# Optimization experiments

Hardware: AMD Instinct MI355X
Metric: run time of the kernel (lower is better)

## Reference

```python
import jax, jax.numpy as jnp
import numpy as np

RES = (32, 32, 32)   # S, H, W
WS = 4               # window size (cubic)
SHIFT = 2            # shift size
NH = 6               # num heads
C = 192              # dim
EPS = 1e-5


def _rel_pos_index(ws):
    coords = np.stack(np.meshgrid(np.arange(ws), np.arange(ws), np.arange(ws), indexing='ij'))
    cf = coords.reshape(3, -1)                      # (3, N)
    rc = (cf[:, :, None] - cf[:, None, :]).transpose(1, 2, 0).astype(np.int64)  # (N,N,3)
    rc[..., 0] += ws - 1
    rc[..., 1] += ws - 1
    rc[..., 2] += ws - 1
    rc[..., 0] *= 3 * ws - 1
    rc[..., 1] *= 2 * ws - 1
    return rc.sum(-1)                               # (N, N)

_RPI = jnp.asarray(_rel_pos_index(WS))


def _ln(x, g, b):
    m = jnp.mean(x, axis=-1, keepdims=True)
    v = jnp.mean(jnp.square(x - m), axis=-1, keepdims=True)
    return (x - m) * jax.lax.rsqrt(v + EPS) * g + b


def setup_inputs():
    key = jax.random.key(0)
    ks = jax.random.split(key, 12)
    B, L = 2, RES[0] * RES[1] * RES[2]
    nW, N = 512, WS ** 3
    Hd = 4 * C
    p = lambda k, s: jax.random.normal(k, s, jnp.float32) * 0.02
    return {
        'x': jax.random.normal(ks[0], (B, L, C), jnp.float32),
        'mask_matrix': jax.random.normal(ks[1], (nW, N, N), jnp.float32),
        'skip': jax.random.normal(ks[2], (B, L, C), jnp.float32),
        'x_up': jax.random.normal(ks[3], (B, L, C), jnp.float32),
        'norm1_g': jnp.ones((C,), jnp.float32), 'norm1_b': jnp.zeros((C,), jnp.float32),
        'kv_w': p(ks[4], (C, 2 * C)), 'kv_b': jnp.zeros((2 * C,), jnp.float32),
        'rpb_table': p(ks[5], ((2 * WS - 1) ** 3, NH)),
        'proj_w': p(ks[6], (C, C)), 'proj_b': jnp.zeros((C,), jnp.float32),
        'norm2_g': jnp.ones((C,), jnp.float32), 'norm2_b': jnp.zeros((C,), jnp.float32),
        'fc1_w': p(ks[7], (C, Hd)), 'fc1_b': jnp.zeros((Hd,), jnp.float32),
        'fc2_w': p(ks[8], (Hd, C)), 'fc2_b': jnp.zeros((C,), jnp.float32),
    }


def reference(x, mask_matrix, skip, x_up, norm1_g, norm1_b, kv_w, kv_b, rpb_table,
              proj_w, proj_b, norm2_g, norm2_b, fc1_w, fc1_b, fc2_w, fc2_b):
    B, L, _ = x.shape
    S, H, W = RES
    ws, N = WS, WS ** 3
    hd = C // NH
    scale = hd ** -0.5

    sn = _ln(skip, norm1_g, norm1_b).reshape(B, S, H, W, C)
    qn = _ln(x_up, norm1_g, norm1_b).reshape(B, S, H, W, C)
    # cyclic shift (shift_size > 0)
    sn = jnp.roll(sn, (-SHIFT, -SHIFT, -SHIFT), axis=(1, 2, 3))
    qn = jnp.roll(qn, (-SHIFT, -SHIFT, -SHIFT), axis=(1, 2, 3))

    def part(t):  # window partition -> (B*nW, N, C)
        t = t.reshape(B, S // ws, ws, H // ws, ws, W // ws, ws, C)
        return t.transpose(0, 1, 3, 5, 2, 4, 6, 7).reshape(-1, N, C)

    skw, qw = part(sn), part(qn)
    B_ = skw.shape[0]

    kv = (skw @ kv_w + kv_b).reshape(B_, N, 2, NH, hd)
    k = kv[:, :, 0].transpose(0, 2, 1, 3)   # (B_, NH, N, hd)
    v = kv[:, :, 1].transpose(0, 2, 1, 3)
    q = qw.reshape(B_, N, NH, hd).transpose(0, 2, 1, 3) * scale

    attn = jnp.einsum('bhqd,bhkd->bhqk', q, k)
    rpb = rpb_table[_RPI.reshape(-1)].reshape(N, N, NH).transpose(2, 0, 1)  # (NH, N, N)
    attn = attn + rpb[None]
    nW = mask_matrix.shape[0]
    attn = attn.reshape(B, nW, NH, N, N) + mask_matrix[None, :, None]
    attn = jax.nn.softmax(attn.reshape(B_, NH, N, N), axis=-1)

    out = jnp.einsum('bhqk,bhkd->bhqd', attn, v).transpose(0, 2, 1, 3).reshape(B_, N, C)
    out = out @ proj_w + proj_b

    # window reverse
    out = out.reshape(B, S // ws, H // ws, W // ws, ws, ws, ws, C)
    out = out.transpose(0, 1, 4, 2, 5, 3, 6, 7).reshape(B, S, H, W, C)
    out = jnp.roll(out, (SHIFT, SHIFT, SHIFT), axis=(1, 2, 3)).reshape(B, L, C)

    x = x + out
    h = _ln(x, norm2_g, norm2_b)
    h = jax.nn.gelu(h @ fc1_w + fc1_b, approximate=False) @ fc2_w + fc2_b
    return x + h
```

## Files before the change

kernel.cpp:

```cpp
#include <hip/hip_runtime.h>
#include <math.h>

typedef unsigned short u16;
typedef __bf16 bf16x8 __attribute__((ext_vector_type(8)));
typedef float f32x4 __attribute__((ext_vector_type(4)));
typedef unsigned short u16x8 __attribute__((ext_vector_type(8)));

#define SHIFT 2

static __device__ __forceinline__ f32x4 mfma16(bf16x8 a, bf16x8 b, f32x4 c) {
  return __builtin_amdgcn_mfma_f32_16x16x32_bf16(a, b, c, 0, 0, 0);
}
static __device__ __forceinline__ u16 f2bf(float f) {
  unsigned u = __builtin_bit_cast(unsigned, f);
  unsigned r = u + 0x7fffu + ((u >> 16) & 1u);
  return (u16)(r >> 16);
}
static __device__ __forceinline__ float bf2f(u16 u) {
  unsigned v = (unsigned)u << 16;
  return __builtin_bit_cast(float, v);
}
static __device__ __forceinline__ void stage16(const u16* g, u16* lbase, int lane) {
#if __has_builtin(__builtin_amdgcn_global_load_lds)
  __builtin_amdgcn_global_load_lds(
      (const __attribute__((address_space(1))) unsigned int*)g,
      (__attribute__((address_space(3))) unsigned int*)lbase, 16, 0, 0);
#else
  *(u16x8*)(lbase + lane * 8) = *(const u16x8*)g;
#endif
}

#define OFF_KVWT  ((size_t)0)
#define OFF_PRWT  (OFF_KVWT + 384*192*2)
#define OFF_FC1WT (OFF_PRWT + 192*192*2)
#define OFF_FC2WT (OFF_FC1WT + 768*192*2)
#define OFF_SKW   (OFF_FC2WT + 192*768*2)
#define OFF_QW    (OFF_SKW + (size_t)65536*192*2)
#define OFF_KVB   (OFF_QW + (size_t)65536*192*2)
#define OFF_HN    (OFF_KVB + (size_t)65536*384*2)
#define OFF_PO    (OFF_HN + (size_t)65536*192*2)

__global__ __launch_bounds__(256) void k_prep(
    const float* __restrict__ kv_w, const float* __restrict__ proj_w,
    const float* __restrict__ fc1_w, const float* __restrict__ fc2_w,
    u16* __restrict__ kvT, u16* __restrict__ prT,
    u16* __restrict__ f1T, u16* __restrict__ f2T) {
  int i = blockIdx.x * 256 + threadIdx.x;
  if (i < 192 * 384) kvT[(i % 384) * 192 + i / 384] = f2bf(kv_w[i]);
  if (i < 192 * 192) prT[(i % 192) * 192 + i / 192] = f2bf(proj_w[i]);
  if (i < 192 * 768) f1T[(i % 768) * 192 + i / 768] = f2bf(fc1_w[i]);
  if (i < 768 * 192) f2T[(i % 192) * 768 + i / 192] = f2bf(fc2_w[i]);
}

__global__ __launch_bounds__(256) void k_ln_part(
    const float* __restrict__ skip, const float* __restrict__ x_up,
    const float* __restrict__ gam, const float* __restrict__ bet,
    u16* __restrict__ skw, u16* __restrict__ qw) {
  int row = blockIdx.x * 4 + (threadIdx.x >> 6);
  int lane = threadIdx.x & 63;
  const float* sp = skip + (size_t)row * 192;
  const float* qp = x_up + (size_t)row * 192;
  float sv[3], qv[3], ss = 0.f, qs = 0.f;
#pragma unroll
  for (int j = 0; j < 3; j++) {
    sv[j] = sp[lane + 64 * j]; qv[j] = qp[lane + 64 * j];
    ss += sv[j]; qs += qv[j];
  }
#pragma unroll
  for (int m = 1; m < 64; m <<= 1) { ss += __shfl_xor(ss, m, 64); qs += __shfl_xor(qs, m, 64); }
  float sm = ss * (1.f / 192.f), qm = qs * (1.f / 192.f);
  float s2 = 0.f, q2 = 0.f;
#pragma unroll
  for (int j = 0; j < 3; j++) { float d = sv[j] - sm; s2 += d * d; d = qv[j] - qm; q2 += d * d; }
#pragma unroll
  for (int m = 1; m < 64; m <<= 1) { s2 += __shfl_xor(s2, m, 64); q2 += __shfl_xor(q2, m, 64); }
  float sr = rsqrtf(s2 * (1.f / 192.f) + 1e-5f), qr = rsqrtf(q2 * (1.f / 192.f) + 1e-5f);
  int b = row >> 15, l = row & 32767;
  int s = l >> 10, h = (l >> 5) & 31, w = l & 31;
  int s_ = (s - SHIFT) & 31, h_ = (h - SHIFT) & 31, w_ = (w - SHIFT) & 31;
  int wIdx = ((s_ >> 2) * 8 + (h_ >> 2)) * 8 + (w_ >> 2);
  int n = ((s_ & 3) * 4 + (h_ & 3)) * 4 + (w_ & 3);
  size_t orow = ((size_t)(b * 512 + wIdx) * 64 + n) * 192;
  const float scale = 0.17677669529663687f;
#pragma unroll
  for (int j = 0; j < 3; j++) {
    int cc = lane + 64 * j;
    float gg = gam[cc], bb = bet[cc];
    skw[orow + cc] = f2bf((sv[j] - sm) * sr * gg + bb);
    qw[orow + cc]  = f2bf(((qv[j] - qm) * qr * gg + bb) * scale);
  }
}

__global__ __launch_bounds__(256) void k_kv(
    const u16* __restrict__ A, const u16* __restrict__ BT,
    const float* __restrict__ bias, u16* __restrict__ outh) {
  __shared__ u16 lds[(128 + 128) * 64];
  int mb = blockIdx.x, nb = blockIdx.y;
  int tid = threadIdx.x, w = tid >> 6, l = tid & 63;
  int wr = w >> 1, wc = w & 1, g = l >> 4, c = l & 15;
  f32x4 acc[4][4] = {};
  for (int ks = 0; ks < 3; ks++) {
    if (ks) __syncthreads();
    int k0 = ks * 64;
#pragma unroll
    for (int i = 0; i < 4; i++) {
      int s = w * 4 + i;
      stage16(&A[(size_t)(mb * 128 + s * 8 + (l >> 3)) * 192 + k0 + (l & 7) * 8],
              &lds[s * 512], l);
      stage16(&BT[(size_t)(nb * 128 + s * 8 + (l >> 3)) * 192 + k0 + (l & 7) * 8],
              &lds[8192 + s * 512], l);
    }
    __syncthreads();
#pragma unroll
    for (int kk = 0; kk < 2; kk++) {
      bf16x8 a[4];
#pragma unroll
      for (int m = 0; m < 4; m++)
        a[m] = *(const bf16x8*)&lds[(wr * 64 + m * 16 + c) * 64 + kk * 32 + g * 8];
#pragma unroll
      for (int n = 0; n < 4; n++) {
        bf16x8 b = *(const bf16x8*)&lds[8192 + (wc * 64 + n * 16 + c) * 64 + kk * 32 + g * 8];
#pragma unroll
        for (int m = 0; m < 4; m++) acc[m][n] = mfma16(a[m], b, acc[m][n]);
      }
    }
  }
#pragma unroll
  for (int m = 0; m < 4; m++)
#pragma unroll
    for (int n = 0; n < 4; n++)
#pragma unroll
      for (int r = 0; r < 4; r++) {
        int row = mb * 128 + wr * 64 + m * 16 + g * 4 + r;
        int col = nb * 128 + wc * 64 + n * 16 + c;
        outh[(size_t)row * 384 + col] = f2bf(acc[m][n][r] + bias[col]);
      }
}

__global__ __launch_bounds__(384) void k_attn_mega(
    const u16* __restrict__ qw, const u16* __restrict__ kvb,
    const float* __restrict__ rpb, const float* __restrict__ mask,
    const u16* __restrict__ prT, const float* __restrict__ proj_b,
    const float* __restrict__ x, const float* __restrict__ g2,
    const float* __restrict__ b2, u16* __restrict__ hn, u16* __restrict__ po) {
  __shared__ u16 lv[64 * 200];
  __shared__ u16 lp[6][16 * 72];
  __shared__ u16 lo[64 * 200];
  __shared__ float pf[64 * 16];
  int b_ = blockIdx.x, wIdx = b_ & 511;
  int tid = threadIdx.x, l = tid & 63, wv = tid >> 6, g = l >> 4, c = l & 15;
#pragma unroll
  for (int i = 0; i < 4; i++) {
    int cid = tid + i * 384;
    int row = cid / 24, ch = cid % 24;
    *(u16x8*)&lv[row * 200 + ch * 8] =
        *(const u16x8*)&kvb[((size_t)b_ * 64 + row) * 384 + 192 + ch * 8];
  }
  __syncthreads();
  int h = wv;
  bf16x8 qa[4], kb[4];
#pragma unroll
  for (int m = 0; m < 4; m++)
    qa[m] = *(const bf16x8*)&qw[((size_t)b_ * 64 + m * 16 + c) * 192 + h * 32 + g * 8];
#pragma unroll
  for (int n = 0; n < 4; n++)
    kb[n] = *(const bf16x8*)&kvb[((size_t)b_ * 64 + n * 16 + c) * 384 + h * 32 + g * 8];
  f32x4 acc[4][4] = {};
#pragma unroll
  for (int m = 0; m < 4; m++)
#pragma unroll
    for (int n = 0; n < 4; n++) acc[m][n] = mfma16(qa[m], kb[n], acc[m][n]);
  bf16x8 vb[2][2];
#pragma unroll
  for (int kk = 0; kk < 2; kk++)
#pragma unroll
    for (int nd = 0; nd < 2; nd++) {
      union { u16 u[8]; bf16x8 v; } bb;
#pragma unroll
      for (int j = 0; j < 8; j++)
        bb.u[j] = lv[(kk * 32 + g * 8 + j) * 200 + h * 32 + nd * 16 + c];
      vb[kk][nd] = bb.v;
    }
  const float* mrow = mask + (size_t)wIdx * 4096;
  f32x4 oacc[4][2] = {};
#pragma unroll
  for (int m = 0; m < 4; m++) {
#pragma unroll
    for (int r = 0; r < 4; r++) {
      int qr = m * 16 + g * 4 + r;
      int qs = qr >> 4, qh = (qr >> 2) & 3, qx = qr & 3;
      float vals[4];
#pragma unroll
      for (int n = 0; n < 4; n++) {
        int kc = n * 16 + c;
        int ks = kc >> 4, kh = (kc >> 2) & 3, kx = kc & 3;
        int idx = (qs - ks + 3) * 11 + (qh - kh + 3) * 7 + (qx - kx + 3);
        vals[n] = acc[m][n][r] + rpb[idx * 6 + h] + mrow[qr * 64 + kc];
      }
      float mx = fmaxf(fmaxf(vals[0], vals[1]), fmaxf(vals[2], vals[3]));
#pragma unroll
      for (int mm = 1; mm < 16; mm <<= 1) mx = fmaxf(mx, __shfl_xor(mx, mm, 64));
      float sum = 0.f;
#pragma unroll
      for (int n = 0; n < 4; n++) { vals[n] = __expf(vals[n] - mx); sum += vals[n]; }
#pragma unroll
      for (int mm = 1; mm < 16; mm <<= 1) sum += __shfl_xor(sum, mm, 64);
      float inv = 1.f / sum;
#pragma unroll
      for (int n = 0; n < 4; n++)
        lp[h][(g * 4 + r) * 72 + n * 16 + c] = f2bf(vals[n] * inv);
    }
#pragma unroll
    for (int kk = 0; kk < 2; kk++) {
      bf16x8 pa = *(const bf16x8*)&lp[h][c * 72 + kk * 32 + g * 8];
#pragma unroll
      for (int nd = 0; nd < 2; nd++) oacc[m][nd] = mfma16(pa, vb[kk][nd], oacc[m][nd]);
    }
  }
#pragma unroll
  for (int m = 0; m < 4; m++)
#pragma unroll
    for (int nd = 0; nd < 2; nd++)
#pragma unroll
      for (int r = 0; r < 4; r++)
        lo[(m * 16 + g * 4 + r) * 200 + h * 32 + nd * 16 + c] = f2bf(oacc[m][nd][r]);
  __syncthreads();
  f32x4 pacc[4][2] = {};
#pragma unroll
  for (int ks = 0; ks < 6; ks++) {
    bf16x8 pa[4];
#pragma unroll
    for (int m = 0; m < 4; m++)
      pa[m] = *(const bf16x8*)&lo[(m * 16 + c) * 200 + ks * 32 + g * 8];
#pragma unroll
    for (int n = 0; n < 2; n++) {
      bf16x8 pb = *(const bf16x8*)&prT[(size_t)(wv * 32 + n * 16 + c) * 192 + ks * 32 + g * 8];
#pragma unroll
      for (int m = 0; m < 4; m++) pacc[m][n] = mfma16(pa[m], pb, pacc[m][n]);
    }
  }
  int bI = b_ >> 9;
  int wS = wIdx >> 6, wH = (wIdx >> 3) & 7, wW = wIdx & 7;
  float yv[4][2][4];
#pragma unroll
  for (int m = 0; m < 4; m++)
#pragma unroll
    for (int r = 0; r < 4; r++) {
      int tok = m * 16 + g * 4 + r;
      int inS = tok >> 4, inH = (tok >> 2) & 3, inW = tok & 3;
      int s = (wS * 4 + inS + SHIFT) & 31;
      int hh = (wH * 4 + inH + SHIFT) & 31;
      int ww = (wW * 4 + inW + SHIFT) & 31;
      size_t base = ((size_t)bI * 32768 + ((size_t)s * 32 + hh) * 32 + ww) * 192;
      float sum = 0.f, sq = 0.f;
#pragma unroll
      for (int n = 0; n < 2; n++) {
        int col = wv * 32 + n * 16 + c;
        float v = pacc[m][n][r] + proj_b[col];
        po[base + col] = f2bf(v);
        float y = v + x[base + col];
        yv[m][n][r] = y;
        sum += y; sq += y * y;
      }
#pragma unroll
      for (int mm = 1; mm < 16; mm <<= 1) { sum += __shfl_xor(sum, mm, 64); sq += __shfl_xor(sq, mm, 64); }
      if (c == 0) { pf[tok * 16 + wv] = sum; pf[tok * 16 + 8 + wv] = sq; }
    }
  __syncthreads();
#pragma unroll
  for (int m = 0; m < 4; m++)
#pragma unroll
    for (int r = 0; r < 4; r++) {
      int tok = m * 16 + g * 4 + r;
      int inS = tok >> 4, inH = (tok >> 2) & 3, inW = tok & 3;
      int s = (wS * 4 + inS + SHIFT) & 31;
      int hh = (wH * 4 + inH + SHIFT) & 31;
      int ww = (wW * 4 + inW + SHIFT) & 31;
      size_t base = ((size_t)bI * 32768 + ((size_t)s * 32 + hh) * 32 + ww) * 192;
      float su = 0.f, qu = 0.f;
#pragma unroll
      for (int w6 = 0; w6 < 6; w6++) { su += pf[tok * 16 + w6]; qu += pf[tok * 16 + 8 + w6]; }
      float mu = su * (1.f / 192.f);
      float rs = rsqrtf(qu * (1.f / 192.f) - mu * mu + 1e-5f);
#pragma unroll
      for (int n = 0; n < 2; n++) {
        int col = wv * 32 + n * 16 + c;
        hn[base + col] = f2bf((yv[m][n][r] - mu) * rs * g2[col] + b2[col]);
      }
    }
}

__global__ __launch_bounds__(256, 2) void k_mlp(
    const u16* __restrict__ hn, const u16* __restrict__ f1T,
    const u16* __restrict__ f2T, const float* __restrict__ b1,
    const float* __restrict__ b2f, const float* __restrict__ x,
    const u16* __restrict__ po, float* __restrict__ out) {
  __shared__ u16 lds[29184];
  u16* f1c = lds;
  u16* f2c = lds + 12288;
  u16* h1c = lds + 24576;
  int tid = threadIdx.x, l = tid & 63, wv = tid >> 6, g = l >> 4, c = l & 15;
  size_t tokbase = (size_t)blockIdx.x * 64;

#pragma unroll
  for (int i = 0; i < 6; i++) {
    int CI = i * 256 + wv * 64 + l;
    int row = CI / 24, chp = CI % 24;
    int sch = (chp & 24) | ((chp ^ row) & 7);
    stage16(hn + (tokbase + row) * 192 + sch * 8, f1c + (i * 256 + wv * 64) * 8, l);
  }
  __syncthreads();
  bf16x8 hb[4][6];
#pragma unroll
  for (int tf = 0; tf < 4; tf++)
#pragma unroll
    for (int ks = 0; ks < 6; ks++) {
      int ch = ks * 4 + g;
      int chp = (ch & 24) | ((ch ^ c) & 7);
      hb[tf][ks] = *(const bf16x8*)&f1c[(tf * 16 + c) * 192 + chp * 8];
    }
  f32x4 acc2[3][4] = {};
#pragma unroll 1
  for (int ko = 0; ko < 12; ko++) {
    __syncthreads();
#pragma unroll
    for (int i = 0; i < 6; i++) {
      int CI = i * 256 + wv * 64 + l;
      int row = CI / 24, chp = CI % 24;
      int sch = (chp & 24) | ((chp ^ row) & 7);
      stage16(f1T + (size_t)(ko * 64 + row) * 192 + sch * 8,
              f1c + (i * 256 + wv * 64) * 8, l);
    }
#pragma unroll
    for (int i = 0; i < 6; i++) {
      int CI = i * 256 + wv * 64 + l;
      int row = CI >> 3, chp = CI & 7;
      int sch = chp ^ (row & 7);
      stage16(f2T + (size_t)row * 768 + ko * 64 + sch * 8,
              f2c + (i * 256 + wv * 64) * 8, l);
    }
    __syncthreads();
    f32x4 acc1[4] = {};
#pragma unroll
    for (int ks = 0; ks < 6; ks++) {
      int ch = ks * 4 + g;
      int chp = (ch & 24) | ((ch ^ c) & 7);
      bf16x8 wa = *(const bf16x8*)&f1c[(wv * 16 + c) * 192 + chp * 8];
#pragma unroll
      for (int tf = 0; tf < 4; tf++) acc1[tf] = mfma16(wa, hb[tf][ks], acc1[tf]);
    }
    float4 b1v = *(const float4*)&b1[ko * 64 + wv * 16 + g * 4];
#pragma unroll
    for (int tf = 0; tf < 4; tf++) {
      unsigned pk[2];
#pragma unroll
      for (int p = 0; p < 2; p++) {
        unsigned lohi[2];
#pragma unroll
        for (int q = 0; q < 2; q++) {
          int r = p * 2 + q;
          float v = acc1[tf][r] + (r == 0 ? b1v.x : r == 1 ? b1v.y : r == 2 ? b1v.z : b1v.w);
          float u2 = v * (1.5957691216f + 0.0713548163f * v * v);
          v = v * (1.f / (1.f + __expf(-u2)));
          lohi[q] = f2bf(v);
        }
        pk[p] = lohi[0] | (lohi[1] << 16);
      }
      *(uint2*)&h1c[(tf * 16 + c) * 72 + wv * 16 + g * 4] = make_uint2(pk[0], pk[1]);
    }
    __syncthreads();
#pragma unroll
    for (int ck = 0; ck < 2; ck++) {
      bf16x8 a2[4];
#pragma unroll
      for (int tf = 0; tf < 4; tf++)
        a2[tf] = *(const bf16x8*)&h1c[(tf * 16 + c) * 72 + ck * 32 + g * 8];
#pragma unroll
      for (int of = 0; of < 3; of++) {
        int ch = ck * 4 + g;
        int chp = ch ^ (c & 7);
        bf16x8 wb = *(const bf16x8*)&f2c[(wv * 48 + of * 16 + c) * 64 + chp * 8];
#pragma unroll
        for (int tf = 0; tf < 4; tf++) acc2[of][tf] = mfma16(a2[tf], wb, acc2[of][tf]);
      }
    }
  }
#pragma unroll
  for (int of = 0; of < 3; of++)
#pragma unroll
    for (int tf = 0; tf < 4; tf++) {
      int col = wv * 48 + of * 16 + c;
      float bb = b2f[col];
#pragma unroll
      for (int r = 0; r < 4; r++) {
        size_t tok = tokbase + tf * 16 + g * 4 + r;
        size_t base = tok * 192 + col;
        out[base] = acc2[of][tf][r] + bb + x[base] + bf2f(po[base]);
      }
    }
}

extern "C" void kernel_launch(void* const* d_in, const int* in_sizes, int n_in,
                              void* d_out, int out_size, void* d_ws, size_t ws_size,
                              hipStream_t stream) {
  const float* x      = (const float*)d_in[0];
  const float* mask   = (const float*)d_in[1];
  const float* skip   = (const float*)d_in[2];
  const float* x_up   = (const float*)d_in[3];
  const float* n1g    = (const float*)d_in[4];
  const float* n1b    = (const float*)d_in[5];
  const float* kv_w   = (const float*)d_in[6];
  const float* kv_b   = (const float*)d_in[7];
  const float* rpb    = (const float*)d_in[8];
  const float* proj_w = (const float*)d_in[9];
  const float* proj_b = (const float*)d_in[10];
  const float* n2g    = (const float*)d_in[11];
  const float* n2b    = (const float*)d_in[12];
  const float* fc1_w  = (const float*)d_in[13];
  const float* fc1_b  = (const float*)d_in[14];
  const float* fc2_w  = (const float*)d_in[15];
  const float* fc2_b  = (const float*)d_in[16];
  char* ws = (char*)d_ws;
  u16* kvT  = (u16*)(ws + OFF_KVWT);
  u16* prT  = (u16*)(ws + OFF_PRWT);
  u16* f1T  = (u16*)(ws + OFF_FC1WT);
  u16* f2T  = (u16*)(ws + OFF_FC2WT);
  u16* skw  = (u16*)(ws + OFF_SKW);
  u16* qw   = (u16*)(ws + OFF_QW);
  u16* kvb  = (u16*)(ws + OFF_KVB);
  u16* hn   = (u16*)(ws + OFF_HN);
  u16* po   = (u16*)(ws + OFF_PO);
  float* out = (float*)d_out;

  k_prep<<<dim3(576), dim3(256), 0, stream>>>(kv_w, proj_w, fc1_w, fc2_w, kvT, prT, f1T, f2T);
  k_ln_part<<<dim3(16384), dim3(256), 0, stream>>>(skip, x_up, n1g, n1b, skw, qw);
  k_kv<<<dim3(512, 3), dim3(256), 0, stream>>>(skw, kvT, kv_b, kvb);
  k_attn_mega<<<dim3(1024), dim3(384), 0, stream>>>(
      qw, kvb, rpb, mask, prT, proj_b, x, n2g, n2b, hn, po);
  k_mlp<<<dim3(1024), dim3(256), 0, stream>>>(hn, f1T, f2T, fc1_b, fc2_b, x, po, out);
}
```

Measured before the change: 270.1 us.

## Retile KV GEMM with full-K weight staging and stage mask/rpb in LDS

The KV projection kernel now stages a full 192x192 weight slab in LDS with an XOR swizzle and streams A fragments straight from global memory, so each block covers 192 output columns and the grid shrinks from 3 to 2 column blocks. In the attention kernel, the per-window mask and the relative-position bias table are cooperatively loaded into LDS instead of being gathered from global memory per element. V is staged with async global-to-LDS loads, and the LDS buffers are aliased to cut the footprint, with launch bounds raised to allow more resident blocks. The added syncs and the larger LDS use in k_kv (72KB) may limit occupancy.

```diff
diff --git a/kernel.cpp b/kernel.cpp
--- a/kernel.cpp
+++ b/kernel.cpp
@@ -91,73 +91,75 @@
   }
 }
 
-__global__ __launch_bounds__(256) void k_kv(
+__global__ __launch_bounds__(256, 2) void k_kv(
     const u16* __restrict__ A, const u16* __restrict__ BT,
     const float* __restrict__ bias, u16* __restrict__ outh) {
-  __shared__ u16 lds[(128 + 128) * 64];
+  __shared__ u16 lw[192 * 192];
   int mb = blockIdx.x, nb = blockIdx.y;
-  int tid = threadIdx.x, w = tid >> 6, l = tid & 63;
-  int wr = w >> 1, wc = w & 1, g = l >> 4, c = l & 15;
-  f32x4 acc[4][4] = {};
-  for (int ks = 0; ks < 3; ks++) {
-    if (ks) __syncthreads();
-    int k0 = ks * 64;
-#pragma unroll
-    for (int i = 0; i < 4; i++) {
-      int s = w * 4 + i;
-      stage16(&A[(size_t)(mb * 128 + s * 8 + (l >> 3)) * 192 + k0 + (l & 7) * 8],
-              &lds[s * 512], l);
-      stage16(&BT[(size_t)(nb * 128 + s * 8 + (l >> 3)) * 192 + k0 + (l & 7) * 8],
-              &lds[8192 + s * 512], l);
-    }
-    __syncthreads();
-#pragma unroll
-    for (int kk = 0; kk < 2; kk++) {
-      bf16x8 a[4];
-#pragma unroll
-      for (int m = 0; m < 4; m++)
-        a[m] = *(const bf16x8*)&lds[(wr * 64 + m * 16 + c) * 64 + kk * 32 + g * 8];
-#pragma unroll
-      for (int n = 0; n < 4; n++) {
-        bf16x8 b = *(const bf16x8*)&lds[8192 + (wc * 64 + n * 16 + c) * 64 + kk * 32 + g * 8];
-#pragma unroll
-        for (int m = 0; m < 4; m++) acc[m][n] = mfma16(a[m], b, acc[m][n]);
-      }
-    }
-  }
-#pragma unroll
-  for (int m = 0; m < 4; m++)
-#pragma unroll
-    for (int n = 0; n < 4; n++)
+  int tid = threadIdx.x, l = tid & 63, wv = tid >> 6, g = l >> 4, c = l & 15;
+  int wr = wv >> 1, wc = wv & 1;
+#pragma unroll
+  for (int i = 0; i < 18; i++) {
+    int CI = i * 256 + tid;
+    int row = CI / 24, ch = CI % 24;
+    int sch = (ch & 24) | ((ch ^ row) & 7);
+    stage16(BT + (size_t)(nb * 192 + row) * 192 + sch * 8, lw + (i * 256 + wv * 64) * 8, l);
+  }
+  __syncthreads();
+  f32x4 acc[4][6] = {};
+#pragma unroll
+  for (int ks = 0; ks < 6; ks++) {
+    bf16x8 a[4];
+#pragma unroll
+    for (int m = 0; m < 4; m++)
+      a[m] = *(const bf16x8*)&A[(size_t)(mb * 128 + wr * 64 + m * 16 + c) * 192 + ks * 32 + g * 8];
+#pragma unroll
+    for (int n = 0; n < 6; n++) {
+      int col = wc * 96 + n * 16 + c;
+      int ch = ks * 4 + g;
+      int chp = (ch & 24) | ((ch ^ col) & 7);
+      bf16x8 b = *(const bf16x8*)&lw[col * 192 + chp * 8];
+#pragma unroll
+      for (int m = 0; m < 4; m++) acc[m][n] = mfma16(a[m], b, acc[m][n]);
+    }
+  }
+#pragma unroll
+  for (int n = 0; n < 6; n++)
+#pragma unroll
+    for (int m = 0; m < 4; m++) {
+      int col = nb * 192 + wc * 96 + n * 16 + c;
+      float bb = bias[col];
 #pragma unroll
       for (int r = 0; r < 4; r++) {
         int row = mb * 128 + wr * 64 + m * 16 + g * 4 + r;
-        int col = nb * 128 + wc * 64 + n * 16 + c;
-        outh[(size_t)row * 384 + col] = f2bf(acc[m][n][r] + bias[col]);
-      }
-}
-
-__global__ __launch_bounds__(384) void k_attn_mega(
+        outh[(size_t)row * 384 + col] = f2bf(acc[m][n][r] + bb);
+      }
+    }
+}
+
+__global__ __launch_bounds__(384, 4) void k_attn_mega(
     const u16* __restrict__ qw, const u16* __restrict__ kvb,
     const float* __restrict__ rpb, const float* __restrict__ mask,
     const u16* __restrict__ prT, const float* __restrict__ proj_b,
     const float* __restrict__ x, const float* __restrict__ g2,
     const float* __restrict__ b2, u16* __restrict__ hn, u16* __restrict__ po) {
-  __shared__ u16 lv[64 * 200];
-  __shared__ u16 lp[6][16 * 72];
-  __shared__ u16 lo[64 * 200];
-  __shared__ float pf[64 * 16];
+  __shared__ __align__(16) char smem[25600 + 13824 + 17408 + 8256];
+  u16* lv = (u16*)smem;
+  u16* lo = (u16*)smem;
+  u16* lp = (u16*)(smem + 25600);
+  float* pf = (float*)(smem + 25600);
+  float* lmaskf = (float*)(smem + 25600 + 13824);
+  float* lrpbf  = (float*)(smem + 25600 + 13824 + 17408);
   int b_ = blockIdx.x, wIdx = b_ & 511;
   int tid = threadIdx.x, l = tid & 63, wv = tid >> 6, g = l >> 4, c = l & 15;
+  int h = wv;
 #pragma unroll
   for (int i = 0; i < 4; i++) {
-    int cid = tid + i * 384;
-    int row = cid / 24, ch = cid % 24;
-    *(u16x8*)&lv[row * 200 + ch * 8] =
-        *(const u16x8*)&kvb[((size_t)b_ * 64 + row) * 384 + 192 + ch * 8];
-  }
-  __syncthreads();
-  int h = wv;
+    int CI = i * 384 + tid;
+    int row = CI / 24, ch = CI % 24;
+    stage16(kvb + ((size_t)b_ * 64 + row) * 384 + 192 + ch * 8,
+            lv + (i * 384 + wv * 64) * 8, l);
+  }
   bf16x8 qa[4], kb[4];
 #pragma unroll
   for (int m = 0; m < 4; m++)
@@ -165,11 +167,22 @@
 #pragma unroll
   for (int n = 0; n < 4; n++)
     kb[n] = *(const bf16x8*)&kvb[((size_t)b_ * 64 + n * 16 + c) * 384 + h * 32 + g * 8];
-  f32x4 acc[4][4] = {};
-#pragma unroll
-  for (int m = 0; m < 4; m++)
-#pragma unroll
-    for (int n = 0; n < 4; n++) acc[m][n] = mfma16(qa[m], kb[n], acc[m][n]);
+  const float* mrow = mask + (size_t)wIdx * 4096;
+#pragma unroll
+  for (int i = 0; i < 3; i++) {
+    int idx = i * 384 + tid;
+    if (idx < 1024) {
+      float4 mv = *(const float4*)&mrow[idx * 4];
+      int row = idx >> 4, c4 = idx & 15;
+      *(float4*)&lmaskf[row * 68 + c4 * 4] = mv;
+    }
+  }
+#pragma unroll
+  for (int i = 0; i < 6; i++) {
+    int idx = i * 384 + tid;
+    if (idx < 2058) lrpbf[idx] = rpb[idx];
+  }
+  __syncthreads();
   bf16x8 vb[2][2];
 #pragma unroll
   for (int kk = 0; kk < 2; kk++)
@@ -178,10 +191,15 @@
       union { u16 u[8]; bf16x8 v; } bb;
 #pragma unroll
       for (int j = 0; j < 8; j++)
-        bb.u[j] = lv[(kk * 32 + g * 8 + j) * 200 + h * 32 + nd * 16 + c];
+        bb.u[j] = lv[(kk * 32 + g * 8 + j) * 192 + h * 32 + nd * 16 + c];
       vb[kk][nd] = bb.v;
     }
-  const float* mrow = mask + (size_t)wIdx * 4096;
+  __syncthreads();
+  f32x4 acc[4][4] = {};
+#pragma unroll
+  for (int m = 0; m < 4; m++)
+#pragma unroll
+    for (int n = 0; n < 4; n++) acc[m][n] = mfma16(qa[m], kb[n], acc[m][n]);
   f32x4 oacc[4][2] = {};
 #pragma unroll
   for (int m = 0; m < 4; m++) {
@@ -195,7 +213,7 @@
         int kc = n * 16 + c;
         int ks = kc >> 4, kh = (kc >> 2) & 3, kx = kc & 3;
         int idx = (qs - ks + 3) * 11 + (qh - kh + 3) * 7 + (qx - kx + 3);
-        vals[n] = acc[m][n][r] + rpb[idx * 6 + h] + mrow[qr * 64 + kc];
+        vals[n] = acc[m][n][r] + lrpbf[idx * 6 + h] + lmaskf[qr * 68 + kc];
       }
       float mx = fmaxf(fmaxf(vals[0], vals[1]), fmaxf(vals[2], vals[3]));
 #pragma unroll
@@ -208,11 +226,11 @@
       float inv = 1.f / sum;
 #pragma unroll
       for (int n = 0; n < 4; n++)
-        lp[h][(g * 4 + r) * 72 + n * 16 + c] = f2bf(vals[n] * inv);
+        lp[h * 1152 + (g * 4 + r) * 72 + n * 16 + c] = f2bf(vals[n] * inv);
     }
 #pragma unroll
     for (int kk = 0; kk < 2; kk++) {
-      bf16x8 pa = *(const bf16x8*)&lp[h][c * 72 + kk * 32 + g * 8];
+      bf16x8 pa = *(const bf16x8*)&lp[h * 1152 + c * 72 + kk * 32 + g * 8];
 #pragma unroll
       for (int nd = 0; nd < 2; nd++) oacc[m][nd] = mfma16(pa, vb[kk][nd], oacc[m][nd]);
     }
@@ -301,7 +319,6 @@
   u16* h1c = lds + 24576;
   int tid = threadIdx.x, l = tid & 63, wv = tid >> 6, g = l >> 4, c = l & 15;
   size_t tokbase = (size_t)blockIdx.x * 64;
-
 #pragma unroll
   for (int i = 0; i < 6; i++) {
     int CI = i * 256 + wv * 64 + l;
@@ -434,7 +451,7 @@
 
   k_prep<<<dim3(576), dim3(256), 0, stream>>>(kv_w, proj_w, fc1_w, fc2_w, kvT, prT, f1T, f2T);
   k_ln_part<<<dim3(16384), dim3(256), 0, stream>>>(skip, x_up, n1g, n1b, skw, qw);
-  k_kv<<<dim3(512, 3), dim3(256), 0, stream>>>(skw, kvT, kv_b, kvb);
+  k_kv<<<dim3(512, 2), dim3(256), 0, stream>>>(skw, kvT, kv_b, kvb);
   k_attn_mega<<<dim3(1024), dim3(384), 0, stream>>>(
       qw, kvb, rpb, mask, prT, proj_b, x, n2g, n2b, hn, po);
   k_mlp<<<dim3(1024), dim3(256), 0, stream>>>(hn, f1T, f2T, fc1_b, fc2_b, x, po, out);
```

Measured after the change: 260.8 us. 3.4% less time.
